# Optimization experiments

Measured on AMD Instinct MI355X. Metric: run time of the kernel, lower is better.

The kernel has to match this reference:

```python
import jax, jax.numpy as jnp
import numpy as np
import math

BS, N = 32, 2048
INPUT_SIZE, HIDDEN, NUM_LAYERS = 128, 64, 4
ALPHA, LAMDA = 0.1, 1.0
EPS = 1e-5
EDGE_P = 0.01


def setup_inputs() -> dict:
    key = jax.random.key(0)
    ks = jax.random.split(key, 6)
    x = jax.random.normal(ks[0], (BS, N, INPUT_SIZE), jnp.float32)
    adj = (jax.random.uniform(ks[1], (BS, N, N)) < EDGE_P).astype(jnp.float32)
    adj = adj * (1.0 - jnp.eye(N, dtype=jnp.float32))  # no pre-existing self loops
    proj_w = jax.random.normal(ks[2], (INPUT_SIZE, HIDDEN), jnp.float32) * (1.0 / math.sqrt(INPUT_SIZE))
    proj_b = jnp.zeros((HIDDEN,), jnp.float32)
    ln_g = jnp.ones((NUM_LAYERS, HIDDEN), jnp.float32)
    ln_b = jnp.zeros((NUM_LAYERS, HIDDEN), jnp.float32)
    conv_w = jax.random.normal(ks[3], (NUM_LAYERS, HIDDEN, HIDDEN), jnp.float32) * (1.0 / math.sqrt(HIDDEN))
    head_w = jax.random.normal(ks[4], (HIDDEN, 1), jnp.float32) * (1.0 / math.sqrt(HIDDEN))
    head_b = jnp.zeros((1,), jnp.float32)
    return dict(x=x, adj=adj, proj_w=proj_w, proj_b=proj_b, ln_g=ln_g, ln_b=ln_b,
                conv_w=conv_w, head_w=head_w, head_b=head_b)


def _layer_norm(h, g, b):
    mu = h.mean(-1, keepdims=True)
    var = ((h - mu) ** 2).mean(-1, keepdims=True)
    return (h - mu) * jax.lax.rsqrt(var + EPS) * g + b


def _gcn_norm(adj):
    # A_hat = D^{-1/2} (A + I) D^{-1/2}; only the nonzero pattern of adj is used,
    # matching adj.nonzero() -> edge_index with unit edge weights + added self loops.
    a = (adj != 0).astype(adj.dtype) + jnp.eye(adj.shape[-1], dtype=adj.dtype)
    dinv = jax.lax.rsqrt(a.sum(-1))  # deg >= 1 thanks to self loops
    return a * dinv[:, :, None] * dinv[:, None, :]


def _forward(x, adj_hat, proj_w, proj_b, ln_g, ln_b, conv_w, head_w, head_b):
    h = x @ proj_w + proj_b  # [bs, N, hidden]
    for i in range(NUM_LAYERS):
        beta = math.log(LAMDA / (i + 1) + 1.0)  # GCNII identity-mapping strength
        # DeepGCNLayer block='res+': h_in -> norm -> act -> conv, then residual add
        z = jax.nn.relu(_layer_norm(h, ln_g[i], ln_b[i]))
        p = jnp.einsum('bij,bjd->bid', adj_hat, z)          # neighbor aggregation
        s = (1.0 - ALPHA) * p + ALPHA * z                   # initial residual (x0 = conv input)
        h = h + (1.0 - beta) * s + beta * (s @ conv_w[i])   # GCN2Conv out + res+ skip
    return h @ head_w + head_b  # [bs, N, 1]


def reference(x, adj, proj_w, proj_b, ln_g, ln_b, conv_w, head_w, head_b):
    return _forward(x, _gcn_norm(adj), proj_w, proj_b, ln_g, ln_b, conv_w, head_w, head_b)
```

## Files before the change

kernel.cpp:

```cpp
#include <hip/hip_runtime.h>
#include <math.h>

#define BS 32
#define N 2048
#define ROWS (BS * N)
#define IN 128
#define HID 64
#define K_CAP 80
#define EPS 1e-5f
#define ALPHA 0.1f

typedef float fx4 __attribute__((ext_vector_type(4)));

__device__ __forceinline__ float bf2f(unsigned short u) {
    union { float f; unsigned v; } x; x.v = ((unsigned)u) << 16; return x.f;
}
__device__ __forceinline__ unsigned short f2bf(float f) {
    union { float f; unsigned v; } x; x.f = f;
    unsigned r = x.v + 0x7fff + ((x.v >> 16) & 1);
    return (unsigned short)(r >> 16);
}

__global__ __launch_bounds__(256) void k_build(const float* __restrict__ adj,
                                               int* __restrict__ ell,
                                               int* __restrict__ cnt,
                                               float* __restrict__ dinv) {
    int lane = threadIdx.x & 63;
    int row  = blockIdx.x * 4 + (threadIdx.x >> 6);
    const fx4* arow = (const fx4*)(adj + (size_t)row * N);
    int* erow = ell + (size_t)row * K_CAP;
    int base = 0;
#pragma unroll
    for (int it = 0; it < N / 256; it++) {
        fx4 f = __builtin_nontemporal_load(&arow[it * 64 + lane]);
#pragma unroll
        for (int k = 0; k < 4; k++) {
            float v = f[k];
            unsigned long long m = __ballot(v != 0.0f);
            if (v != 0.0f) {
                int pos = base + __popcll(m & ((1ull << lane) - 1ull));
                if (pos < K_CAP) erow[pos] = it * 256 + lane * 4 + k;
            }
            base += __popcll(m);
        }
    }
    if (lane == 0) {
        cnt[row]  = base < K_CAP ? base : K_CAP;
        dinv[row] = rsqrtf((float)base + 1.0f);
    }
}

__global__ __launch_bounds__(256) void k_proj_ln(const float* __restrict__ x,
                                                 const float* __restrict__ w,
                                                 const float* __restrict__ b,
                                                 const float* __restrict__ g0,
                                                 const float* __restrict__ b0,
                                                 float* __restrict__ h,
                                                 unsigned short* __restrict__ z0) {
    __shared__ float sw[IN * HID];
    __shared__ float sx[4][IN];
    int tx = threadIdx.x;
    for (int i = tx; i < IN * HID; i += 256) sw[i] = w[i];
    int row0 = blockIdx.x * 4;
    if (tx < 128) {
        float4 v = *(const float4*)(x + (size_t)(row0 + (tx >> 5)) * IN + (tx & 31) * 4);
        *(float4*)&sx[tx >> 5][(tx & 31) * 4] = v;
    }
    __syncthreads();
    int c = tx & 63, r = tx >> 6;
    float acc = b[c];
#pragma unroll
    for (int k = 0; k < IN; k += 4) {
        float4 xa = *(const float4*)&sx[r][k];
        acc += xa.x * sw[(k + 0) * HID + c];
        acc += xa.y * sw[(k + 1) * HID + c];
        acc += xa.z * sw[(k + 2) * HID + c];
        acc += xa.w * sw[(k + 3) * HID + c];
    }
    size_t idx = (size_t)(row0 + r) * HID + c;
    h[idx] = acc;
    float sum = acc;
    for (int o = 32; o >= 1; o >>= 1) sum += __shfl_xor(sum, o);
    float mu = sum * (1.0f / 64.0f);
    float d  = acc - mu;
    float vs = d * d;
    for (int o = 32; o >= 1; o >>= 1) vs += __shfl_xor(vs, o);
    float rr = rsqrtf(vs * (1.0f / 64.0f) + EPS);
    float zz = d * rr * g0[c] + b0[c];
    z0[idx] = f2bf(zz > 0.0f ? zz : 0.0f);
}

__global__ __launch_bounds__(256) void k_layer(
    float* __restrict__ h, const unsigned short* __restrict__ z_in,
    unsigned short* __restrict__ z_out,
    const int* __restrict__ ell, const int* __restrict__ cnt,
    const float* __restrict__ dinv, const float* __restrict__ w,
    const float* __restrict__ g_next, const float* __restrict__ b_next,
    float beta, int is_last,
    const float* __restrict__ head_w, const float* __restrict__ head_b,
    float* __restrict__ out) {
    __shared__ float sw[HID * HID];
    __shared__ float ss[16][HID];
    int tx = threadIdx.x;
    int lane = tx & 63, wid = tx >> 6;
    int p = lane & 15, q = lane >> 4;

    int bid = blockIdx.x;
    int swz = (bid & 7) * (int)(gridDim.x >> 3) + (bid >> 3);
    int row0 = swz * 16 + wid * 4;
    int jbase = row0 & ~(N - 1);

    for (int i = tx; i < HID * HID; i += 256) sw[i] = w[i];

    int   nn[4];
    float di[4];
    int   myidx[4];
    float myw[4];
    float4 zi4[4];
#pragma unroll
    for (int rr = 0; rr < 4; rr++) {
        int row = row0 + rr;
        nn[rr] = cnt[row];
        di[rr] = dinv[row];
        ushort4 zu = *(const ushort4*)(z_in + (size_t)row * HID + 4 * p);
        zi4[rr] = make_float4(bf2f(zu.x), bf2f(zu.y), bf2f(zu.z), bf2f(zu.w));
        myidx[rr] = 0; myw[rr] = 0.0f;
        if (lane < nn[rr]) {
            myidx[rr] = ell[(size_t)row * K_CAP + lane];
            myw[rr]   = dinv[jbase + myidx[rr]];
        }
    }

    float4 acc[4];
#pragma unroll
    for (int rr = 0; rr < 4; rr++) acc[rr] = make_float4(0.f, 0.f, 0.f, 0.f);
    int ntm = 0;
#pragma unroll
    for (int rr = 0; rr < 4; rr++) {
        int nm = nn[rr] < 64 ? nn[rr] : 64;
        nm = (nm + 3) & ~3;
        ntm = nm > ntm ? nm : ntm;
    }
    for (int t = q; t < ntm; t += 4) {
#pragma unroll
        for (int rr = 0; rr < 4; rr++) {
            int   j  = jbase + __shfl(myidx[rr], t);
            float wj = __shfl(myw[rr], t);
            ushort4 zu = *(const ushort4*)(z_in + (size_t)j * HID + 4 * p);
            acc[rr].x += wj * bf2f(zu.x); acc[rr].y += wj * bf2f(zu.y);
            acc[rr].z += wj * bf2f(zu.z); acc[rr].w += wj * bf2f(zu.w);
        }
    }
#pragma unroll
    for (int rr = 0; rr < 4; rr++) {
        for (int t = 64 + q; t < nn[rr]; t += 4) {
            int   j  = jbase + ell[(size_t)(row0 + rr) * K_CAP + t];
            float wj = dinv[j];
            ushort4 zu = *(const ushort4*)(z_in + (size_t)j * HID + 4 * p);
            acc[rr].x += wj * bf2f(zu.x); acc[rr].y += wj * bf2f(zu.y);
            acc[rr].z += wj * bf2f(zu.z); acc[rr].w += wj * bf2f(zu.w);
        }
    }
#pragma unroll
    for (int rr = 0; rr < 4; rr++) {
        float4 a = acc[rr];
        a.x += __shfl_xor(a.x, 16); a.y += __shfl_xor(a.y, 16);
        a.z += __shfl_xor(a.z, 16); a.w += __shfl_xor(a.w, 16);
        a.x += __shfl_xor(a.x, 32); a.y += __shfl_xor(a.y, 32);
        a.z += __shfl_xor(a.z, 32); a.w += __shfl_xor(a.w, 32);
        float dd = di[rr];
        float4 s4;
        s4.x = (1.0f - ALPHA) * dd * (a.x + dd * zi4[rr].x) + ALPHA * zi4[rr].x;
        s4.y = (1.0f - ALPHA) * dd * (a.y + dd * zi4[rr].y) + ALPHA * zi4[rr].y;
        s4.z = (1.0f - ALPHA) * dd * (a.z + dd * zi4[rr].z) + ALPHA * zi4[rr].z;
        s4.w = (1.0f - ALPHA) * dd * (a.w + dd * zi4[rr].w) + ALPHA * zi4[rr].w;
        if (q == 0) *(float4*)&ss[wid * 4 + rr][4 * p] = s4;
    }
    __syncthreads();

#pragma unroll
    for (int rr = 0; rr < 4; rr++) {
        int row = row0 + rr;
        float mv = 0.0f;
#pragma unroll
        for (int k = 0; k < HID; k += 4) {
            float4 sk = *(const float4*)&ss[wid * 4 + rr][k];
            mv += sk.x * sw[(k + 0) * HID + lane];
            mv += sk.y * sw[(k + 1) * HID + lane];
            mv += sk.z * sw[(k + 2) * HID + lane];
            mv += sk.w * sw[(k + 3) * HID + lane];
        }
        float s_c = ss[wid * 4 + rr][lane];
        size_t idx = (size_t)row * HID + lane;
        float hn = __builtin_nontemporal_load(h + idx) +
                   (1.0f - beta) * s_c + beta * mv;
        if (!is_last) {
            __builtin_nontemporal_store(hn, h + idx);
            float sum = hn;
            for (int o = 32; o >= 1; o >>= 1) sum += __shfl_xor(sum, o);
            float mu = sum * (1.0f / 64.0f);
            float d  = hn - mu;
            float vs = d * d;
            for (int o = 32; o >= 1; o >>= 1) vs += __shfl_xor(vs, o);
            float rv = rsqrtf(vs * (1.0f / 64.0f) + EPS);
            float zz = d * rv * g_next[lane] + b_next[lane];
            z_out[idx] = f2bf(zz > 0.0f ? zz : 0.0f);
        } else {
            float v = hn * head_w[lane];
            for (int o = 32; o >= 1; o >>= 1) v += __shfl_xor(v, o);
            if (lane == 0) out[row] = v + head_b[0];
        }
    }
}

extern "C" void kernel_launch(void* const* d_in, const int* in_sizes, int n_in,
                              void* d_out, int out_size, void* d_ws, size_t ws_size,
                              hipStream_t stream) {
    const float* x      = (const float*)d_in[0];
    const float* adj    = (const float*)d_in[1];
    const float* proj_w = (const float*)d_in[2];
    const float* proj_b = (const float*)d_in[3];
    const float* ln_g   = (const float*)d_in[4];
    const float* ln_b   = (const float*)d_in[5];
    const float* conv_w = (const float*)d_in[6];
    const float* head_w = (const float*)d_in[7];
    const float* head_b = (const float*)d_in[8];
    float* out = (float*)d_out;

    float* h  = (float*)d_ws;
    unsigned short* za = (unsigned short*)(h + (size_t)ROWS * HID);
    unsigned short* zb = za + (size_t)ROWS * HID;
    float* dinv = (float*)(zb + (size_t)ROWS * HID);
    int*   cnt  = (int*)(dinv + ROWS);
    int*   ell  = cnt + ROWS;

    dim3 blk(256);

    k_build<<<dim3(ROWS / 4), blk, 0, stream>>>(adj, ell, cnt, dinv);
    k_proj_ln<<<dim3(ROWS / 4), blk, 0, stream>>>(x, proj_w, proj_b, ln_g, ln_b, h, za);

    unsigned short* zin = za;
    unsigned short* zout = zb;
    for (int i = 0; i < 4; i++) {
        float beta = (float)log(1.0 / (double)(i + 1) + 1.0);
        int last = (i == 3);
        int gi = (i + 1) < 3 ? (i + 1) : 3;
        k_layer<<<dim3(ROWS / 16), blk, 0, stream>>>(h, zin, zout, ell, cnt, dinv,
                                                     conv_w + (size_t)i * HID * HID,
                                                     ln_g + gi * HID, ln_b + gi * HID,
                                                     beta, last, head_w, head_b, out);
        unsigned short* t = zin; zin = zout; zout = t;
    }
}
```

Measured before the change: 399.9 us.

## Precompute edge weights, keep conv weights in registers, assign one row per lane group

A new kernel precomputes the normalized edge weights dinv_i*dinv_j and the self-loop weight dinv_i^2 once, so the four layer kernels no longer gather dinv per neighbor or rescale per row. In each layer kernel, each 16-lane group now walks one row's neighbor list serially instead of four lane groups splitting the neighbors of four rows, which removes the cross-group shuffle reduction and the block barrier. The 64x64 conv weight column is loaded into per-thread registers instead of being staged through 16KB of LDS per block. In exchange it adds an extra kernel plus a weight buffer read, raises register pressure (which may reduce occupancy), and puts the gather loads into a serial per-row loop.

```diff
diff --git a/kernel.cpp b/kernel.cpp
--- a/kernel.cpp
+++ b/kernel.cpp
@@ -48,6 +48,21 @@
         cnt[row]  = base < K_CAP ? base : K_CAP;
         dinv[row] = rsqrtf((float)base + 1.0f);
     }
+}
+
+__global__ __launch_bounds__(256) void k_weights(const int* __restrict__ ell,
+                                                 const int* __restrict__ cnt,
+                                                 const float* __restrict__ dinv,
+                                                 float* __restrict__ wgt,
+                                                 float* __restrict__ dself) {
+    int lane = threadIdx.x & 63;
+    int row  = blockIdx.x * 4 + (threadIdx.x >> 6);
+    int jb   = row & ~(N - 1);
+    int n    = cnt[row];
+    float di = dinv[row];
+    for (int t = lane; t < n; t += 64)
+        wgt[(size_t)row * K_CAP + t] = di * dinv[jb + ell[(size_t)row * K_CAP + t]];
+    if (lane == 0) dself[row] = di * di;
 }
 
 __global__ __launch_bounds__(256) void k_proj_ln(const float* __restrict__ x,
@@ -93,13 +108,13 @@
 __global__ __launch_bounds__(256) void k_layer(
     float* __restrict__ h, const unsigned short* __restrict__ z_in,
     unsigned short* __restrict__ z_out,
-    const int* __restrict__ ell, const int* __restrict__ cnt,
-    const float* __restrict__ dinv, const float* __restrict__ w,
+    const int* __restrict__ ell, const float* __restrict__ wgt,
+    const int* __restrict__ cnt, const float* __restrict__ dself,
+    const float* __restrict__ w,
     const float* __restrict__ g_next, const float* __restrict__ b_next,
     float beta, int is_last,
     const float* __restrict__ head_w, const float* __restrict__ head_b,
     float* __restrict__ out) {
-    __shared__ float sw[HID * HID];
     __shared__ float ss[16][HID];
     int tx = threadIdx.x;
     int lane = tx & 63, wid = tx >> 6;
@@ -110,73 +125,34 @@
     int row0 = swz * 16 + wid * 4;
     int jbase = row0 & ~(N - 1);
 
-    for (int i = tx; i < HID * HID; i += 256) sw[i] = w[i];
-
-    int   nn[4];
-    float di[4];
-    int   myidx[4];
-    float myw[4];
-    float4 zi4[4];
-#pragma unroll
-    for (int rr = 0; rr < 4; rr++) {
-        int row = row0 + rr;
-        nn[rr] = cnt[row];
-        di[rr] = dinv[row];
-        ushort4 zu = *(const ushort4*)(z_in + (size_t)row * HID + 4 * p);
-        zi4[rr] = make_float4(bf2f(zu.x), bf2f(zu.y), bf2f(zu.z), bf2f(zu.w));
-        myidx[rr] = 0; myw[rr] = 0.0f;
-        if (lane < nn[rr]) {
-            myidx[rr] = ell[(size_t)row * K_CAP + lane];
-            myw[rr]   = dinv[jbase + myidx[rr]];
-        }
-    }
-
-    float4 acc[4];
-#pragma unroll
-    for (int rr = 0; rr < 4; rr++) acc[rr] = make_float4(0.f, 0.f, 0.f, 0.f);
-    int ntm = 0;
-#pragma unroll
-    for (int rr = 0; rr < 4; rr++) {
-        int nm = nn[rr] < 64 ? nn[rr] : 64;
-        nm = (nm + 3) & ~3;
-        ntm = nm > ntm ? nm : ntm;
-    }
-    for (int t = q; t < ntm; t += 4) {
-#pragma unroll
-        for (int rr = 0; rr < 4; rr++) {
-            int   j  = jbase + __shfl(myidx[rr], t);
-            float wj = __shfl(myw[rr], t);
-            ushort4 zu = *(const ushort4*)(z_in + (size_t)j * HID + 4 * p);
-            acc[rr].x += wj * bf2f(zu.x); acc[rr].y += wj * bf2f(zu.y);
-            acc[rr].z += wj * bf2f(zu.z); acc[rr].w += wj * bf2f(zu.w);
-        }
-    }
-#pragma unroll
-    for (int rr = 0; rr < 4; rr++) {
-        for (int t = 64 + q; t < nn[rr]; t += 4) {
-            int   j  = jbase + ell[(size_t)(row0 + rr) * K_CAP + t];
-            float wj = dinv[j];
-            ushort4 zu = *(const ushort4*)(z_in + (size_t)j * HID + 4 * p);
-            acc[rr].x += wj * bf2f(zu.x); acc[rr].y += wj * bf2f(zu.y);
-            acc[rr].z += wj * bf2f(zu.z); acc[rr].w += wj * bf2f(zu.w);
-        }
-    }
-#pragma unroll
-    for (int rr = 0; rr < 4; rr++) {
-        float4 a = acc[rr];
-        a.x += __shfl_xor(a.x, 16); a.y += __shfl_xor(a.y, 16);
-        a.z += __shfl_xor(a.z, 16); a.w += __shfl_xor(a.w, 16);
-        a.x += __shfl_xor(a.x, 32); a.y += __shfl_xor(a.y, 32);
-        a.z += __shfl_xor(a.z, 32); a.w += __shfl_xor(a.w, 32);
-        float dd = di[rr];
+    float wcol[HID];
+#pragma unroll
+    for (int k = 0; k < HID; k++) wcol[k] = w[k * HID + lane];
+
+    {
+        int row = row0 + q;
+        int n = cnt[row];
+        float ds = dself[row];
+        const int*   erow = ell + (size_t)row * K_CAP;
+        const float* wrow = wgt + (size_t)row * K_CAP;
+        ushort4 zu0 = *(const ushort4*)(z_in + (size_t)row * HID + 4 * p);
+        float4 zi4 = make_float4(bf2f(zu0.x), bf2f(zu0.y), bf2f(zu0.z), bf2f(zu0.w));
+        float4 acc = make_float4(0.f, 0.f, 0.f, 0.f);
+#pragma unroll 2
+        for (int t = 0; t < n; t++) {
+            int   j  = erow[t];
+            float wj = wrow[t];
+            ushort4 zu = *(const ushort4*)(z_in + (size_t)(jbase + j) * HID + 4 * p);
+            acc.x += wj * bf2f(zu.x); acc.y += wj * bf2f(zu.y);
+            acc.z += wj * bf2f(zu.z); acc.w += wj * bf2f(zu.w);
+        }
         float4 s4;
-        s4.x = (1.0f - ALPHA) * dd * (a.x + dd * zi4[rr].x) + ALPHA * zi4[rr].x;
-        s4.y = (1.0f - ALPHA) * dd * (a.y + dd * zi4[rr].y) + ALPHA * zi4[rr].y;
-        s4.z = (1.0f - ALPHA) * dd * (a.z + dd * zi4[rr].z) + ALPHA * zi4[rr].z;
-        s4.w = (1.0f - ALPHA) * dd * (a.w + dd * zi4[rr].w) + ALPHA * zi4[rr].w;
-        if (q == 0) *(float4*)&ss[wid * 4 + rr][4 * p] = s4;
-    }
-    __syncthreads();
+        s4.x = (1.0f - ALPHA) * (acc.x + ds * zi4.x) + ALPHA * zi4.x;
+        s4.y = (1.0f - ALPHA) * (acc.y + ds * zi4.y) + ALPHA * zi4.y;
+        s4.z = (1.0f - ALPHA) * (acc.z + ds * zi4.z) + ALPHA * zi4.z;
+        s4.w = (1.0f - ALPHA) * (acc.w + ds * zi4.w) + ALPHA * zi4.w;
+        *(float4*)&ss[wid * 4 + q][4 * p] = s4;
+    }
 
 #pragma unroll
     for (int rr = 0; rr < 4; rr++) {
@@ -185,10 +161,8 @@
 #pragma unroll
         for (int k = 0; k < HID; k += 4) {
             float4 sk = *(const float4*)&ss[wid * 4 + rr][k];
-            mv += sk.x * sw[(k + 0) * HID + lane];
-            mv += sk.y * sw[(k + 1) * HID + lane];
-            mv += sk.z * sw[(k + 2) * HID + lane];
-            mv += sk.w * sw[(k + 3) * HID + lane];
+            mv += sk.x * wcol[k] + sk.y * wcol[k + 1] +
+                  sk.z * wcol[k + 2] + sk.w * wcol[k + 3];
         }
         float s_c = ss[wid * 4 + rr][lane];
         size_t idx = (size_t)row * HID + lane;
@@ -230,13 +204,16 @@
     float* h  = (float*)d_ws;
     unsigned short* za = (unsigned short*)(h + (size_t)ROWS * HID);
     unsigned short* zb = za + (size_t)ROWS * HID;
-    float* dinv = (float*)(zb + (size_t)ROWS * HID);
-    int*   cnt  = (int*)(dinv + ROWS);
-    int*   ell  = cnt + ROWS;
+    float* dinv  = (float*)(zb + (size_t)ROWS * HID);
+    float* dself = dinv + ROWS;
+    int*   cnt   = (int*)(dself + ROWS);
+    int*   ell   = cnt + ROWS;
+    float* wgt   = (float*)(ell + (size_t)ROWS * K_CAP);
 
     dim3 blk(256);
 
     k_build<<<dim3(ROWS / 4), blk, 0, stream>>>(adj, ell, cnt, dinv);
+    k_weights<<<dim3(ROWS / 4), blk, 0, stream>>>(ell, cnt, dinv, wgt, dself);
     k_proj_ln<<<dim3(ROWS / 4), blk, 0, stream>>>(x, proj_w, proj_b, ln_g, ln_b, h, za);
 
     unsigned short* zin = za;
@@ -245,7 +222,7 @@
         float beta = (float)log(1.0 / (double)(i + 1) + 1.0);
         int last = (i == 3);
         int gi = (i + 1) < 3 ? (i + 1) : 3;
-        k_layer<<<dim3(ROWS / 16), blk, 0, stream>>>(h, zin, zout, ell, cnt, dinv,
+        k_layer<<<dim3(ROWS / 16), blk, 0, stream>>>(h, zin, zout, ell, wgt, cnt, dself,
                                                      conv_w + (size_t)i * HID * HID,
                                                      ln_g + gi * HID, ln_b + gi * HID,
                                                      beta, last, head_w, head_b, out);
```

After: 431.0 us. 7.8% more time.

## Drop shared weight staging in layer kernel; read weights from global per wave

Applied to the files above, without the earlier changes.

Removes the 16KB shared-memory copy of the conv weight and the block-wide barrier. Each wave now reads the weight columns straight from global/L2 and computes all four row matvecs in one pass over k. The neighbor weight dinv is now looked up inside the gather loop instead of being preloaded and shuffled, and gather addressing uses a per-batch base pointer. This cuts LDS footprint and synchronization, which may raise occupancy, at the cost of more global loads for weights and dinv. It relies on each wave reading only its own ss rows, so skipping the barrier is safe only within a wavefront.

```diff
diff --git a/kernel.cpp b/kernel.cpp
--- a/kernel.cpp
+++ b/kernel.cpp
@@ -77,7 +77,8 @@
         acc += xa.z * sw[(k + 2) * HID + c];
         acc += xa.w * sw[(k + 3) * HID + c];
     }
-    size_t idx = (size_t)(row0 + r) * HID + c;
+    size_t idx = (size_t)(row0 + r) * IN / 2 + c;
+    idx = (size_t)(row0 + r) * HID + c;
     h[idx] = acc;
     float sum = acc;
     for (int o = 32; o >= 1; o >>= 1) sum += __shfl_xor(sum, o);
@@ -99,7 +100,6 @@
     float beta, int is_last,
     const float* __restrict__ head_w, const float* __restrict__ head_b,
     float* __restrict__ out) {
-    __shared__ float sw[HID * HID];
     __shared__ float ss[16][HID];
     int tx = threadIdx.x;
     int lane = tx & 63, wid = tx >> 6;
@@ -109,26 +109,20 @@
     int swz = (bid & 7) * (int)(gridDim.x >> 3) + (bid >> 3);
     int row0 = swz * 16 + wid * 4;
     int jbase = row0 & ~(N - 1);
-
-    for (int i = tx; i < HID * HID; i += 256) sw[i] = w[i];
+    const unsigned short* zbat = z_in + ((size_t)jbase << 6);
 
     int   nn[4];
     float di[4];
     int   myidx[4];
-    float myw[4];
     float4 zi4[4];
 #pragma unroll
     for (int rr = 0; rr < 4; rr++) {
         int row = row0 + rr;
         nn[rr] = cnt[row];
         di[rr] = dinv[row];
-        ushort4 zu = *(const ushort4*)(z_in + (size_t)row * HID + 4 * p);
+        ushort4 zu = *(const ushort4*)(z_in + ((size_t)row << 6) + 4 * p);
         zi4[rr] = make_float4(bf2f(zu.x), bf2f(zu.y), bf2f(zu.z), bf2f(zu.w));
-        myidx[rr] = 0; myw[rr] = 0.0f;
-        if (lane < nn[rr]) {
-            myidx[rr] = ell[(size_t)row * K_CAP + lane];
-            myw[rr]   = dinv[jbase + myidx[rr]];
-        }
+        myidx[rr] = (lane < nn[rr]) ? ell[(size_t)row * K_CAP + lane] : 0;
     }
 
     float4 acc[4];
@@ -144,9 +138,9 @@
     for (int t = q; t < ntm; t += 4) {
 #pragma unroll
         for (int rr = 0; rr < 4; rr++) {
-            int   j  = jbase + __shfl(myidx[rr], t);
-            float wj = __shfl(myw[rr], t);
-            ushort4 zu = *(const ushort4*)(z_in + (size_t)j * HID + 4 * p);
+            int   j  = __shfl(myidx[rr], t);
+            float wj = (t < nn[rr]) ? dinv[jbase + j] : 0.0f;
+            ushort4 zu = *(const ushort4*)(zbat + ((size_t)j << 6) + 4 * p);
             acc[rr].x += wj * bf2f(zu.x); acc[rr].y += wj * bf2f(zu.y);
             acc[rr].z += wj * bf2f(zu.z); acc[rr].w += wj * bf2f(zu.w);
         }
@@ -156,7 +150,7 @@
         for (int t = 64 + q; t < nn[rr]; t += 4) {
             int   j  = jbase + ell[(size_t)(row0 + rr) * K_CAP + t];
             float wj = dinv[j];
-            ushort4 zu = *(const ushort4*)(z_in + (size_t)j * HID + 4 * p);
+            ushort4 zu = *(const ushort4*)(z_in + ((size_t)j << 6) + 4 * p);
             acc[rr].x += wj * bf2f(zu.x); acc[rr].y += wj * bf2f(zu.y);
             acc[rr].z += wj * bf2f(zu.z); acc[rr].w += wj * bf2f(zu.w);
         }
@@ -176,24 +170,28 @@
         s4.w = (1.0f - ALPHA) * dd * (a.w + dd * zi4[rr].w) + ALPHA * zi4[rr].w;
         if (q == 0) *(float4*)&ss[wid * 4 + rr][4 * p] = s4;
     }
-    __syncthreads();
+
+    float mv[4] = {0.f, 0.f, 0.f, 0.f};
+#pragma unroll
+    for (int k = 0; k < HID; k += 4) {
+        float w0 = w[(k + 0) * HID + lane];
+        float w1 = w[(k + 1) * HID + lane];
+        float w2 = w[(k + 2) * HID + lane];
+        float w3 = w[(k + 3) * HID + lane];
+#pragma unroll
+        for (int rr = 0; rr < 4; rr++) {
+            float4 sk = *(const float4*)&ss[wid * 4 + rr][k];
+            mv[rr] += sk.x * w0 + sk.y * w1 + sk.z * w2 + sk.w * w3;
+        }
+    }
 
 #pragma unroll
     for (int rr = 0; rr < 4; rr++) {
         int row = row0 + rr;
-        float mv = 0.0f;
-#pragma unroll
-        for (int k = 0; k < HID; k += 4) {
-            float4 sk = *(const float4*)&ss[wid * 4 + rr][k];
-            mv += sk.x * sw[(k + 0) * HID + lane];
-            mv += sk.y * sw[(k + 1) * HID + lane];
-            mv += sk.z * sw[(k + 2) * HID + lane];
-            mv += sk.w * sw[(k + 3) * HID + lane];
-        }
         float s_c = ss[wid * 4 + rr][lane];
         size_t idx = (size_t)row * HID + lane;
         float hn = __builtin_nontemporal_load(h + idx) +
-                   (1.0f - beta) * s_c + beta * mv;
+                   (1.0f - beta) * s_c + beta * mv[rr];
         if (!is_last) {
             __builtin_nontemporal_store(hn, h + idx);
             float sum = hn;
```

New measurement: 791.5 us. 1.98x slower.
